# Kernel optimization log

Measured on AMD Instinct MI355X. Metric: run time of the kernel, lower is better.

## Reference

```python
import jax, jax.numpy as jnp
import numpy as np

B, H, W, D = 4, 64, 64, 384
M, P = 12, 9
DH = D // M             # 32 head dim
DFF = 3 * D             # 1152 FFN hidden
N = H * W               # 4096 queries (single level)


def setup_inputs():
    key = jax.random.key(0)
    ks = jax.random.split(key, 12)
    g = lambda k, s, sc=0.02: jax.random.normal(k, s, jnp.float32) * sc
    return {
        "x": jax.random.normal(ks[0], (B, D, H, W), jnp.float32),
        "qry_masks": jnp.zeros((B, H, W), jnp.float32),
        "so_w": g(ks[1], (M * P * 2, D)), "so_b": g(ks[2], (M * P * 2,)),
        "aw_w": g(ks[3], (M * P, D)), "aw_b": g(ks[4], (M * P,)),
        "vp_w": g(ks[5], (D, D)), "vp_b": jnp.zeros((D,), jnp.float32),
        "op_w": g(ks[6], (D, D)), "op_b": jnp.zeros((D,), jnp.float32),
        "ln1_g": jnp.ones((D,), jnp.float32), "ln1_b": jnp.zeros((D,), jnp.float32),
        "w1": g(ks[7], (DFF, D)), "w2": g(ks[8], (D, DFF)),
        "ln2_g": jnp.ones((D,), jnp.float32), "ln2_b": jnp.zeros((D,), jnp.float32),
        "level_embed": g(ks[9], (1, D), 1.0),
    }


def _layernorm(x, g, b, eps=1e-5):
    mu = x.mean(-1, keepdims=True)
    v = ((x - mu) ** 2).mean(-1, keepdims=True)
    return (x - mu) * jax.lax.rsqrt(v + eps) * g + b


def _sine_pos(mask):
    # mask: [B,H,W] bool. mmdet SinePositionalEncoding(num_feats=D//2, normalize=True)
    not_mask = (~mask).astype(jnp.float32)
    y = jnp.cumsum(not_mask, 1)
    x = jnp.cumsum(not_mask, 2)
    eps, scale = 1e-6, 2.0 * np.pi
    y = y / (y[:, -1:, :] + eps) * scale
    x = x / (x[:, :, -1:] + eps) * scale
    nf = D // 2
    dim_t = 10000.0 ** (2.0 * (jnp.arange(nf) // 2).astype(jnp.float32) / nf)
    px, py = x[..., None] / dim_t, y[..., None] / dim_t

    def interleave(p):
        return jnp.stack([jnp.sin(p[..., 0::2]), jnp.cos(p[..., 1::2])], -1).reshape(p.shape[:-1] + (nf,))

    return jnp.concatenate([interleave(py), interleave(px)], -1)  # [B,H,W,D]


def _bilinear_gather(v, px, py):
    # v: [B,M,HW,DH]; px,py: [B,M,NP] pixel coords (grid_sample align_corners=False, zero pad)
    x0 = jnp.floor(px); y0 = jnp.floor(py)
    lx, ly = px - x0, py - y0
    x0i, y0i = x0.astype(jnp.int32), y0.astype(jnp.int32)
    out = jnp.zeros(v.shape[:2] + (px.shape[-1], v.shape[-1]), v.dtype)
    for dx, dy, wgt in ((0, 0, (1 - lx) * (1 - ly)), (1, 0, lx * (1 - ly)),
                        (0, 1, (1 - lx) * ly), (1, 1, lx * ly)):
        xi, yi = x0i + dx, y0i + dy
        valid = ((xi >= 0) & (xi < W) & (yi >= 0) & (yi < H)).astype(v.dtype)
        idx = jnp.clip(yi, 0, H - 1) * W + jnp.clip(xi, 0, W - 1)
        g = jnp.take_along_axis(v, idx[..., None], axis=2)  # [B,M,NP,DH]
        out = out + (wgt * valid)[..., None] * g
    return out


def _msdeform_attn(q, value_in, ref, mask_flat,
                   so_w, so_b, aw_w, aw_b, vp_w, vp_b, op_w, op_b):
    value = value_in @ vp_w.T + vp_b                      # [B,N,D]
    value = jnp.where(mask_flat[..., None], 0.0, value)
    so = (q @ so_w.T + so_b).reshape(B, N, M, P, 2)       # single level
    aw = jax.nn.softmax((q @ aw_w.T + aw_b).reshape(B, N, M, P), axis=-1)
    norm = jnp.array([W, H], jnp.float32)
    loc = ref[:, :, None, None, :] + so / norm            # [B,N,M,P,2] in [0,1]
    v = value.reshape(B, N, M, DH).transpose(0, 2, 1, 3)  # [B,M,HW,DH]
    px = (loc[..., 0] * W - 0.5).transpose(0, 2, 1, 3).reshape(B, M, N * P)
    py = (loc[..., 1] * H - 0.5).transpose(0, 2, 1, 3).reshape(B, M, N * P)
    sampled = _bilinear_gather(v, px, py).reshape(B, M, N, P, DH)
    out = jnp.einsum('bmnpd,bnmp->bnmd', sampled, aw).reshape(B, N, D)
    return out @ op_w.T + op_b


def reference(x, qry_masks, so_w, so_b, aw_w, aw_b, vp_w, vp_b, op_w, op_b,
              ln1_g, ln1_b, w1, w2, ln2_g, ln2_b, level_embed):
    mask = (qry_masks == 255.0)                           # [B,H,W] bool
    pos = _sine_pos(mask).reshape(B, N, D) + level_embed[0]
    src = x.reshape(B, D, N).transpose(0, 2, 1)           # [B,N,D]
    mask_flat = mask.reshape(B, N)
    gy, gx = jnp.meshgrid((jnp.arange(H, dtype=jnp.float32) + 0.5) / H,
                          (jnp.arange(W, dtype=jnp.float32) + 0.5) / W, indexing='ij')
    ref = jnp.stack([gx.reshape(-1), gy.reshape(-1)], -1)[None]  # [1,N,2] (x,y)
    q = src
    attn = _msdeform_attn(q + pos, q, ref, mask_flat,
                          so_w, so_b, aw_w, aw_b, vp_w, vp_b, op_w, op_b)
    q = _layernorm(q + attn, ln1_g, ln1_b)
    q = _layernorm(q + jax.nn.relu(q @ w1.T) @ w2.T, ln2_g, ln2_b)
    return q.transpose(0, 2, 1).reshape(B, D, H, W)
```

## Files before the change

kernel.cpp:

```cpp
#include <hip/hip_runtime.h>
#include <math.h>

#define Bc   4
#define Hc   64
#define Wc   64
#define Dc   384
#define Nc   4096
#define Mc   12
#define Pc   9
#define DHc  32
#define DFFc 1152
#define BNc  (Bc*Nc)

typedef __attribute__((ext_vector_type(8))) short short8;
typedef __attribute__((ext_vector_type(4))) float floatx4;

__device__ __forceinline__ ushort f2bf(float f) {
    union { float f; unsigned u; } v; v.f = f;
    unsigned r = v.u + 0x7fffu + ((v.u >> 16) & 1u);
    return (ushort)(r >> 16);
}
__device__ __forceinline__ float bf2f(ushort u) {
    union { unsigned u; float f; } v; v.u = (unsigned)u << 16; return v.f;
}

__device__ __forceinline__ void gload_lds16(const void* g, void* l) {
    __builtin_amdgcn_global_load_lds(
        (const __attribute__((address_space(1))) void*)(uintptr_t)g,
        (__attribute__((address_space(3))) void*)(uintptr_t)l,
        16, 0, 0);
}

#define SOW_N  82944
#define AWW_N  41472
#define VPW_N  147456
#define OPW_N  147456
#define W1_N   442368
#define W2_N   442368
#define WTOT   1304064

__global__ void init_kernel(const float* __restrict__ so_w,
                            const float* __restrict__ aw_w,
                            const float* __restrict__ vp_w,
                            const float* __restrict__ op_w,
                            const float* __restrict__ w1,
                            const float* __restrict__ w2,
                            const float* __restrict__ so_b,
                            const float* __restrict__ aw_b,
                            ushort* __restrict__ out,
                            float* __restrict__ bias_out) {
    int i = blockIdx.x * 256 + threadIdx.x;
    if (i < WTOT) {
        float v;
        int j = i;
        if (j < SOW_N) v = so_w[j];
        else if ((j -= SOW_N) < AWW_N) v = aw_w[j];
        else if ((j -= AWW_N) < VPW_N) v = vp_w[j];
        else if ((j -= VPW_N) < OPW_N) v = op_w[j];
        else if ((j -= OPW_N) < W1_N)  v = w1[j];
        else { j -= W1_N; v = w2[j]; }
        out[i] = f2bf(v);
        return;
    }
    int j = i - WTOT;
    if (j < 384) {
        bias_out[j] = (j < 216) ? so_b[j] : (j < 324 ? aw_b[j - 216] : 0.f);
    }
}

__global__ __launch_bounds__(256) void cumsum_kernel(
        const float* __restrict__ qmask,
        float* __restrict__ cum_y, float* __restrict__ cum_x) {
    __shared__ float nm[64 * 65];
    __shared__ float ot[64 * 65];
    int b = blockIdx.x;
    int t = threadIdx.x;
    const float* qm = qmask + b * 4096;
    #pragma unroll
    for (int k = 0; k < 16; ++k) {
        int idx = t + k * 256;
        nm[(idx >> 6) * 65 + (idx & 63)] = (qm[idx] == 255.0f) ? 0.f : 1.f;
    }
    __syncthreads();
    if (t < 64) {
        float run = 0.f;
        for (int h = 0; h < 64; ++h) { run += nm[h * 65 + t]; ot[h * 65 + t] = run; }
    }
    __syncthreads();
    #pragma unroll
    for (int k = 0; k < 16; ++k) {
        int idx = t + k * 256;
        cum_y[b * 4096 + idx] = ot[(idx >> 6) * 65 + (idx & 63)];
    }
    __syncthreads();
    if (t < 64) {
        float run = 0.f;
        for (int w = 0; w < 64; ++w) { run += nm[t * 65 + w]; ot[t * 65 + w] = run; }
    }
    __syncthreads();
    #pragma unroll
    for (int k = 0; k < 16; ++k) {
        int idx = t + k * 256;
        cum_x[b * 4096 + idx] = ot[(idx >> 6) * 65 + (idx & 63)];
    }
}

__global__ void transpose_pos_kernel(const float* __restrict__ x,
                                     const float* __restrict__ cum_y,
                                     const float* __restrict__ cum_x,
                                     const float* __restrict__ level_embed,
                                     ushort* __restrict__ src_bf,
                                     ushort* __restrict__ qpos_bf) {
    __shared__ float tile[32][33];
    int b  = blockIdx.z;
    int n0 = blockIdx.x * 32, d0 = blockIdx.y * 32;
    int tx = threadIdx.x, ty = threadIdx.y;
    tile[ty][tx] = x[((size_t)b * Dc + (d0 + ty)) * Nc + (n0 + tx)];
    __syncthreads();
    int n = n0 + ty, d = d0 + tx;
    float v = tile[tx][ty];
    size_t oi = ((size_t)b * Nc + n) * Dc + d;
    src_bf[oi] = f2bf(v);
    int h = n >> 6, w = n & 63;
    const float TWO_PI = 6.28318530717958647692f;
    float vy = cum_y[(b * Hc + h) * Wc + w] /
               (cum_y[(b * Hc + (Hc - 1)) * Wc + w] + 1e-6f) * TWO_PI;
    float vx = cum_x[(b * Hc + h) * Wc + w] /
               (cum_x[(b * Hc + h) * Wc + (Wc - 1)] + 1e-6f) * TWO_PI;
    int   i  = (d < 192) ? d : d - 192;
    float vv = (d < 192) ? vy : vx;
    float e   = (float)(i >> 1) * (2.0f / 192.0f);
    float idt = exp2f(e * -13.28771237954945f);
    float ang = vv * idt;
    float pe  = (i & 1) ? __cosf(ang) : __sinf(ang);
    qpos_bf[oi] = f2bf(v + pe + level_embed[d]);
}

template <int KT>
__device__ __forceinline__ void gemm_core(
        const ushort* __restrict__ A, const ushort* __restrict__ Wt,
        const float* __restrict__ bias,
        float* __restrict__ Cf, ushort* __restrict__ Cb,
        int Nout, int relu, const float* __restrict__ qmask,
        ushort* As, ushort* Bs) {
    constexpr int NCH = KT / 32;
    const int tid  = threadIdx.x;
    const int m0   = blockIdx.x * 128;
    const int n0   = blockIdx.y * 128;
    const int lane = tid & 63;
    const int wv   = tid >> 6;
    const int wr   = (wv >> 1) * 64;
    const int wc   = (wv & 1) * 64;
    const int quad = lane >> 4;
    const int lrow = lane & 15;
    const int srow = wv * 32 + (lane >> 2);
    const int scol = (lane & 3) * 8;

    floatx4 acc[4][4];
    #pragma unroll
    for (int i = 0; i < 4; ++i)
        #pragma unroll
        for (int j = 0; j < 4; ++j)
            acc[i][j] = (floatx4)(0.f);

    #pragma unroll
    for (int s = 0; s < 2; ++s) {
        gload_lds16(A  + (size_t)(m0 + srow + s * 16) * KT + scol,
                    As + wv * 1024 + s * 512);
        gload_lds16(Wt + (size_t)(n0 + srow + s * 16) * KT + scol,
                    Bs + wv * 1024 + s * 512);
    }

    for (int c = 0; c < NCH; ++c) {
        const int cur = c & 1;
        __syncthreads();
        if (c + 1 < NCH) {
            const int k0 = (c + 1) * 32;
            #pragma unroll
            for (int s = 0; s < 2; ++s) {
                gload_lds16(A  + (size_t)(m0 + srow + s * 16) * KT + k0 + scol,
                            As + (cur ^ 1) * 4096 + wv * 1024 + s * 512);
                gload_lds16(Wt + (size_t)(n0 + srow + s * 16) * KT + k0 + scol,
                            Bs + (cur ^ 1) * 4096 + wv * 1024 + s * 512);
            }
        }
        short8 afr[4], bfr[4];
        #pragma unroll
        for (int i = 0; i < 4; ++i)
            afr[i] = *(const short8*)(As + cur * 4096 +
                                      (wr + i * 16 + lrow) * 32 + quad * 8);
        #pragma unroll
        for (int j = 0; j < 4; ++j)
            bfr[j] = *(const short8*)(Bs + cur * 4096 +
                                      (wc + j * 16 + lrow) * 32 + quad * 8);
        #pragma unroll
        for (int i = 0; i < 4; ++i)
            #pragma unroll
            for (int j = 0; j < 4; ++j)
                acc[i][j] = __builtin_amdgcn_mfma_f32_16x16x32_bf16(
                    afr[i], bfr[j], acc[i][j], 0, 0, 0);
    }

    float mz[4][4];
    #pragma unroll
    for (int i = 0; i < 4; ++i)
        #pragma unroll
        for (int r = 0; r < 4; ++r) {
            int row = m0 + wr + i * 16 + quad * 4 + r;
            mz[i][r] = (qmask && qmask[row] == 255.0f) ? 0.f : 1.f;
        }

    #pragma unroll
    for (int i = 0; i < 4; ++i) {
        #pragma unroll
        for (int j = 0; j < 4; ++j) {
            int col = n0 + wc + j * 16 + lrow;
            if (col >= Nout) continue;
            float bsv = bias ? bias[col] : 0.f;
            #pragma unroll
            for (int r = 0; r < 4; ++r) {
                int row = m0 + wr + i * 16 + quad * 4 + r;
                float v = acc[i][j][r] + bsv;
                if (relu) v = fmaxf(v, 0.f);
                v *= mz[i][r];
                if (Cf) Cf[(size_t)row * Nout + col] = v;
                if (Cb) Cb[(size_t)row * Nout + col] = f2bf(v);
            }
        }
    }
}

__global__ __launch_bounds__(256) void gemm_dual_kernel(
        const ushort* __restrict__ A0, const ushort* __restrict__ W0,
        const float* __restrict__ b0, float* __restrict__ Cf0,
        const ushort* __restrict__ A1, const ushort* __restrict__ W1,
        const float* __restrict__ b1, ushort* __restrict__ Cb1,
        const float* __restrict__ qmask) {
    __shared__ ushort As[2 * 128 * 32];
    __shared__ ushort Bs[2 * 128 * 32];
    if (blockIdx.z == 0)
        gemm_core<384>(A0, W0, b0, Cf0, nullptr, 384, 0, nullptr, As, Bs);
    else
        gemm_core<384>(A1, W1, b1, nullptr, Cb1, 384, 0, qmask, As, Bs);
}

template <int KT>
__global__ __launch_bounds__(512) void gemm_fullrow_kernel(
        const ushort* __restrict__ A, const ushort* __restrict__ Wt,
        const float* __restrict__ bias, const void* __restrict__ resid,
        const float* __restrict__ g, const float* __restrict__ beta,
        float* __restrict__ outf, ushort* __restrict__ outb) {
    constexpr int NCH = KT / 32;
    __shared__ ushort As[4 * 2048];
    __shared__ ushort Bs[4 * 12288];
    __shared__ float eps1[8][64], eps2[8][64];
    __shared__ float mu_l[64], rs_l[64];
    const int tid  = threadIdx.x;
    const int lane = tid & 63;
    const int wv   = tid >> 6;
    const int quad = lane >> 4;
    const int lrow = lane & 15;
    const int m0   = blockIdx.x * 64;
    const int srow = lane >> 2;
    const int scol = (lane & 3) * 8;

    floatx4 acc[4][3];
    #pragma unroll
    for (int i = 0; i < 4; ++i)
        #pragma unroll
        for (int j = 0; j < 3; ++j)
            acc[i][j] = (floatx4)(0.f);

#define STAGE_CHUNK(c, buf)                                                   \
    {   const int k0_ = (c) * 32;                                             \
        if (wv < 4)                                                           \
            gload_lds16(A + (size_t)(m0 + wv * 16 + srow) * KT + k0_ + scol,  \
                        As + (buf) * 2048 + wv * 512);                        \
        _Pragma("unroll")                                                     \
        for (int s_ = 0; s_ < 3; ++s_)                                        \
            gload_lds16(Wt + (size_t)(wv * 48 + s_ * 16 + srow) * KT + k0_ + scol, \
                        Bs + (buf) * 12288 + wv * 1536 + s_ * 512);           \
    }

    STAGE_CHUNK(0, 0)
    STAGE_CHUNK(1, 1)
    STAGE_CHUNK(2, 2)

    #pragma unroll
    for (int c = 0; c < NCH; ++c) {
        const int rem = (NCH - 1 - c) >= 2 ? 2 : (NCH - 1 - c);
        if (wv < 4) {
            if (rem == 2)      asm volatile("s_waitcnt vmcnt(8)" ::: "memory");
            else if (rem == 1) asm volatile("s_waitcnt vmcnt(4)" ::: "memory");
            else               asm volatile("s_waitcnt vmcnt(0)" ::: "memory");
        } else {
            if (rem == 2)      asm volatile("s_waitcnt vmcnt(6)" ::: "memory");
            else if (rem == 1) asm volatile("s_waitcnt vmcnt(3)" ::: "memory");
            else               asm volatile("s_waitcnt vmcnt(0)" ::: "memory");
        }
        __builtin_amdgcn_s_barrier();
        __builtin_amdgcn_sched_barrier(0);
        if (c + 3 < NCH) { STAGE_CHUNK(c + 3, (c + 3) & 3) }
        const int buf = c & 3;
        short8 afr[4], bfr[3];
        #pragma unroll
        for (int i = 0; i < 4; ++i)
            afr[i] = *(const short8*)(As + buf * 2048 +
                                      (i * 16 + lrow) * 32 + quad * 8);
        #pragma unroll
        for (int j = 0; j < 3; ++j)
            bfr[j] = *(const short8*)(Bs + buf * 12288 +
                                      (wv * 48 + j * 16 + lrow) * 32 + quad * 8);
        #pragma unroll
        for (int i = 0; i < 4; ++i)
            #pragma unroll
            for (int j = 0; j < 3; ++j)
                acc[i][j] = __builtin_amdgcn_mfma_f32_16x16x32_bf16(
                    afr[i], bfr[j], acc[i][j], 0, 0, 0);
    }
#undef STAGE_CHUNK

    float s1[16], s2[16];
    #pragma unroll
    for (int k = 0; k < 16; ++k) { s1[k] = 0.f; s2[k] = 0.f; }
    #pragma unroll
    for (int i = 0; i < 4; ++i) {
        #pragma unroll
        for (int r = 0; r < 4; ++r) {
            int rl = i * 16 + quad * 4 + r;
            #pragma unroll
            for (int j = 0; j < 3; ++j) {
                int col = wv * 48 + j * 16 + lrow;
                float t = acc[i][j][r];
                if (bias) t += bias[col];
                t += bf2f(((const ushort*)resid)[(size_t)(m0 + rl) * Dc + col]);
                acc[i][j][r] = t;
                s1[i * 4 + r] += t;
                s2[i * 4 + r] += t * t;
            }
        }
    }
    #pragma unroll
    for (int mm = 1; mm < 16; mm <<= 1) {
        #pragma unroll
        for (int k = 0; k < 16; ++k) {
            s1[k] += __shfl_xor(s1[k], mm);
            s2[k] += __shfl_xor(s2[k], mm);
        }
    }
    if (lrow == 0) {
        #pragma unroll
        for (int i = 0; i < 4; ++i)
            #pragma unroll
            for (int r = 0; r < 4; ++r) {
                int rl = i * 16 + quad * 4 + r;
                eps1[wv][rl] = s1[i * 4 + r];
                eps2[wv][rl] = s2[i * 4 + r];
            }
    }
    __syncthreads();
    if (tid < 64) {
        float a1 = 0.f, a2 = 0.f;
        #pragma unroll
        for (int w = 0; w < 8; ++w) { a1 += eps1[w][tid]; a2 += eps2[w][tid]; }
        float mu  = a1 * (1.0f / Dc);
        float var = a2 * (1.0f / Dc) - mu * mu;
        mu_l[tid] = mu;
        rs_l[tid] = rsqrtf(var + 1e-5f);
    }
    __syncthreads();
    #pragma unroll
    for (int i = 0; i < 4; ++i) {
        #pragma unroll
        for (int r = 0; r < 4; ++r) {
            int rl = i * 16 + quad * 4 + r;
            float mu = mu_l[rl], rs = rs_l[rl];
            #pragma unroll
            for (int j = 0; j < 3; ++j) {
                int col = wv * 48 + j * 16 + lrow;
                float v = (acc[i][j][r] - mu) * rs * g[col] + beta[col];
                outf[(size_t)(m0 + rl) * Dc + col] = v;
                outb[(size_t)(m0 + rl) * Dc + col] = f2bf(v);
            }
        }
    }
}

__global__ __launch_bounds__(512) void ffn_fused_kernel(
        const ushort* __restrict__ A,
        const ushort* __restrict__ W1b,
        const ushort* __restrict__ W2b,
        const float* __restrict__ resid,
        const float* __restrict__ g, const float* __restrict__ beta,
        float* __restrict__ outf) {
    __shared__ ushort smem[69632];
    ushort* Ast = smem;
    ushort* Hs  = smem + 24576;
    ushort* W1s = smem + 32768;
    ushort* W2s = smem + 45056;
    __shared__ float eps1[8][64], eps2[8][64];
    __shared__ float mu_l[64], rs_l[64];

    const int tid  = threadIdx.x;
    const int lane = tid & 63;
    const int wv   = tid >> 6;
    const int quad = lane >> 4;
    const int lrow = lane & 15;
    const int m0   = blockIdx.x * 64;
    const int srow = lane >> 2;
    const int scol = (lane & 3) * 8;

    ushort* W1w = W1s + wv * 1536;
    ushort* W2w = W2s + wv * 3072;

    floatx4 acc2[4][3];
    #pragma unroll
    for (int i = 0; i < 4; ++i)
        #pragma unroll
        for (int j = 0; j < 3; ++j)
            acc2[i][j] = (floatx4)(0.f);

#define STAGE_W1(hcv, kcv, buf)                                               \
    gload_lds16(W1b + (size_t)((hcv) * 128 + wv * 16 + srow) * 384 + (kcv) * 32 + scol, \
                W1w + (buf) * 512 + lane * 8);

#define STAGE_W2(hcv, kc2v, buf)                                              \
    _Pragma("unroll")                                                         \
    for (int s_ = 0; s_ < 3; ++s_)                                            \
        gload_lds16(W2b + (size_t)(wv * 48 + s_ * 16 + srow) * 1152 + (hcv) * 128 + (kc2v) * 32 + scol, \
                    W2w + (buf) * 1536 + s_ * 512 + lane * 8);

    #pragma unroll
    for (int k = 0; k < 6; ++k) {
        int l   = tid + 512 * k;
        int kc_ = l >> 8;
        int rem = l & 255;
        gload_lds16(A + (size_t)(m0 + (rem >> 2)) * 384 + kc_ * 32 + (rem & 3) * 8,
                    Ast + l * 8);
    }
    STAGE_W1(0, 0, 0)
    STAGE_W1(0, 1, 1)
    asm volatile("s_waitcnt vmcnt(2)" ::: "memory");
    __builtin_amdgcn_sched_barrier(0);
    __builtin_amdgcn_s_barrier();
    __builtin_amdgcn_sched_barrier(0);

    floatx4 acc1[4];
    for (int hc = 0; hc < 9; ++hc) {
        #pragma unroll
        for (int i = 0; i < 4; ++i) acc1[i] = (floatx4)(0.f);

        #pragma unroll
        for (int kc = 0; kc < 12; ++kc) {
            if (kc < 10)      { STAGE_W1(hc, kc + 2, (kc + 2) % 3) }
            else if (kc == 10){ STAGE_W2(hc, 0, 0) }
            else              { STAGE_W2(hc, 1, 1) }
            if (kc < 10)       asm volatile("s_waitcnt vmcnt(2)" ::: "memory");
            else if (kc == 10) asm volatile("s_waitcnt vmcnt(4)" ::: "memory");
            else               asm volatile("s_waitcnt vmcnt(6)" ::: "memory");
            short8 afr[4], bfr;
            #pragma unroll
            for (int i = 0; i < 4; ++i)
                afr[i] = *(const short8*)(Ast + kc * 2048 +
                                          (i * 16 + lrow) * 32 + quad * 8);
            bfr = *(const short8*)(W1w + (kc % 3) * 512 + lrow * 32 + quad * 8);
            #pragma unroll
            for (int i = 0; i < 4; ++i)
                acc1[i] = __builtin_amdgcn_mfma_f32_16x16x32_bf16(
                    afr[i], bfr, acc1[i], 0, 0, 0);
        }

        #pragma unroll
        for (int i = 0; i < 4; ++i)
            #pragma unroll
            for (int r = 0; r < 4; ++r) {
                int row = i * 16 + quad * 4 + r;
                Hs[(wv >> 1) * 2048 + row * 32 + (wv & 1) * 16 + lrow] =
                    f2bf(fmaxf(acc1[i][r], 0.f));
            }
        asm volatile("s_waitcnt lgkmcnt(0)" ::: "memory");
        __builtin_amdgcn_sched_barrier(0);
        __builtin_amdgcn_s_barrier();
        __builtin_amdgcn_sched_barrier(0);

        #pragma unroll
        for (int kc2 = 0; kc2 < 4; ++kc2) {
            if (kc2 == 0)      asm volatile("s_waitcnt vmcnt(3)" ::: "memory");
            else if (kc2 == 1) asm volatile("s_waitcnt vmcnt(4)" ::: "memory");
            else if (kc2 == 2) asm volatile("s_waitcnt vmcnt(5)" ::: "memory");
            else               asm volatile("s_waitcnt vmcnt(1)" ::: "memory");
            short8 afr[4], bfr[3];
            #pragma unroll
            for (int i = 0; i < 4; ++i)
                afr[i] = *(const short8*)(Hs + kc2 * 2048 +
                                          (i * 16 + lrow) * 32 + quad * 8);
            #pragma unroll
            for (int j = 0; j < 3; ++j)
                bfr[j] = *(const short8*)(W2w + (kc2 & 1) * 1536 +
                                          (j * 16 + lrow) * 32 + quad * 8);
            asm volatile("s_waitcnt lgkmcnt(0)" ::: "memory");
            __builtin_amdgcn_sched_barrier(0);
            if (kc2 == 0)      { STAGE_W2(hc, 2, 0) STAGE_W1(hc + 1, 0, 0) }
            else if (kc2 == 1) { STAGE_W2(hc, 3, 1) STAGE_W1(hc + 1, 1, 1) }
            #pragma unroll
            for (int i = 0; i < 4; ++i)
                #pragma unroll
                for (int j = 0; j < 3; ++j)
                    acc2[i][j] = __builtin_amdgcn_mfma_f32_16x16x32_bf16(
                        afr[i], bfr[j], acc2[i][j], 0, 0, 0);
        }
        asm volatile("s_waitcnt lgkmcnt(0)" ::: "memory");
        __builtin_amdgcn_sched_barrier(0);
        __builtin_amdgcn_s_barrier();
        __builtin_amdgcn_sched_barrier(0);
    }
    asm volatile("s_waitcnt vmcnt(0)" ::: "memory");
#undef STAGE_W1
#undef STAGE_W2

    float s1[16], s2[16];
    #pragma unroll
    for (int k = 0; k < 16; ++k) { s1[k] = 0.f; s2[k] = 0.f; }
    #pragma unroll
    for (int i = 0; i < 4; ++i) {
        #pragma unroll
        for (int r = 0; r < 4; ++r) {
            int rl = i * 16 + quad * 4 + r;
            #pragma unroll
            for (int j = 0; j < 3; ++j) {
                int col = wv * 48 + j * 16 + lrow;
                float t = acc2[i][j][r];
                t += resid[(size_t)(m0 + rl) * Dc + col];
                acc2[i][j][r] = t;
                s1[i * 4 + r] += t;
                s2[i * 4 + r] += t * t;
            }
        }
    }
    #pragma unroll
    for (int mm = 1; mm < 16; mm <<= 1) {
        #pragma unroll
        for (int k = 0; k < 16; ++k) {
            s1[k] += __shfl_xor(s1[k], mm);
            s2[k] += __shfl_xor(s2[k], mm);
        }
    }
    if (lrow == 0) {
        #pragma unroll
        for (int i = 0; i < 4; ++i)
            #pragma unroll
            for (int r = 0; r < 4; ++r) {
                int rl = i * 16 + quad * 4 + r;
                eps1[wv][rl] = s1[i * 4 + r];
                eps2[wv][rl] = s2[i * 4 + r];
            }
    }
    __syncthreads();
    if (tid < 64) {
        float a1 = 0.f, a2 = 0.f;
        #pragma unroll
        for (int w = 0; w < 8; ++w) { a1 += eps1[w][tid]; a2 += eps2[w][tid]; }
        float mu  = a1 * (1.0f / Dc);
        float var = a2 * (1.0f / Dc) - mu * mu;
        mu_l[tid] = mu;
        rs_l[tid] = rsqrtf(var + 1e-5f);
    }
    __syncthreads();
    #pragma unroll
    for (int i = 0; i < 4; ++i) {
        #pragma unroll
        for (int r = 0; r < 4; ++r) {
            int rl = i * 16 + quad * 4 + r;
            float mu = mu_l[rl], rs = rs_l[rl];
            #pragma unroll
            for (int j = 0; j < 3; ++j) {
                int col = wv * 48 + j * 16 + lrow;
                acc2[i][j][r] = (acc2[i][j][r] - mu) * rs * g[col] + beta[col];
            }
        }
    }
    float* tile = (float*)smem;
    const int b   = m0 >> 12;
    const int n0r = m0 & 4095;
    #pragma unroll
    for (int gp = 0; gp < 2; ++gp) {
        __syncthreads();
        if ((wv >> 2) == gp) {
            int cbase = (wv & 3) * 48;
            #pragma unroll
            for (int i = 0; i < 4; ++i)
                #pragma unroll
                for (int j = 0; j < 3; ++j) {
                    int c = cbase + j * 16 + lrow;
                    #pragma unroll
                    for (int r = 0; r < 4; ++r) {
                        int rl = i * 16 + quad * 4 + r;
                        tile[rl * 193 + c] = acc2[i][j][r];
                    }
                }
        }
        __syncthreads();
        const int row = tid & 63;
        const int cp  = tid >> 6;
        #pragma unroll
        for (int it = 0; it < 24; ++it) {
            int c = it * 8 + cp;
            outf[((size_t)(b * Dc + gp * 192 + c)) * Nc + n0r + row] =
                tile[row * 193 + c];
        }
    }
}

__global__ __launch_bounds__(256) void deform_attn_kernel(
        const ushort* __restrict__ value_bf, const float* __restrict__ soaw,
        ushort* __restrict__ out) {
    int bid   = blockIdx.x;
    int slice = bid % 48;
    int h     = bid / 48;
    int m  = slice % Mc;
    int b  = slice / Mc;
    int w  = threadIdx.x >> 2;
    int l4 = threadIdx.x & 3;
    int n  = (h << 6) | w;
    int bn = b * Nc + n;
    const float* sop = soaw + (size_t)bn * 384 + m * 18;
    const float* lgt = soaw + (size_t)bn * 384 + 216 + m * Pc;
    float awv[Pc];
    float mx = lgt[0];
    #pragma unroll
    for (int i = 1; i < Pc; ++i) mx = fmaxf(mx, lgt[i]);
    float ssum = 0.f;
    #pragma unroll
    for (int i = 0; i < Pc; ++i) { awv[i] = __expf(lgt[i] - mx); ssum += awv[i]; }
    float sinv = 1.f / ssum;
    const ushort* vb = value_bf + ((size_t)b * Nc) * Dc + m * DHc + l4 * 8;
    float acc[8] = {0.f, 0.f, 0.f, 0.f, 0.f, 0.f, 0.f, 0.f};
    #pragma unroll
    for (int p = 0; p < Pc; ++p) {
        float2 so2 = *(const float2*)(sop + p * 2);
        float px = (float)w + so2.x;
        float py = (float)h + so2.y;
        float x0f = floorf(px), y0f = floorf(py);
        float lx = px - x0f, ly = py - y0f;
        int x0 = (int)x0f, y0 = (int)y0f;
        int x1 = x0 + 1,  y1 = y0 + 1;
        float a = awv[p] * sinv;
        float w00 = (1.f - lx) * (1.f - ly) * a;
        float w01 = lx * (1.f - ly) * a;
        float w10 = (1.f - lx) * ly * a;
        float w11 = lx * ly * a;
        bool bx0 = (unsigned)x0 < 64u, bx1 = (unsigned)x1 < 64u;
        bool by0 = (unsigned)y0 < 64u, by1 = (unsigned)y1 < 64u;
        w00 = (bx0 && by0) ? w00 : 0.f;
        w01 = (bx1 && by0) ? w01 : 0.f;
        w10 = (bx0 && by1) ? w10 : 0.f;
        w11 = (bx1 && by1) ? w11 : 0.f;
        int cx0 = min(max(x0, 0), 63), cx1 = min(max(x1, 0), 63);
        int cy0 = min(max(y0, 0), 63), cy1 = min(max(y1, 0), 63);
        uint4 q00 = *(const uint4*)(vb + (size_t)(cy0 * 64 + cx0) * Dc);
        uint4 q01 = *(const uint4*)(vb + (size_t)(cy0 * 64 + cx1) * Dc);
        uint4 q10 = *(const uint4*)(vb + (size_t)(cy1 * 64 + cx0) * Dc);
        uint4 q11 = *(const uint4*)(vb + (size_t)(cy1 * 64 + cx1) * Dc);
        union { unsigned u; float f; } t;
        #define ACC2(word, wg, k)                                   \
            t.u = (word) << 16;         acc[k]     += (wg) * t.f;   \
            t.u = (word) & 0xffff0000u; acc[k + 1] += (wg) * t.f;
        #define ACC8(q, wg) \
            ACC2((q).x, wg, 0) ACC2((q).y, wg, 2) ACC2((q).z, wg, 4) ACC2((q).w, wg, 6)
        ACC8(q00, w00) ACC8(q01, w01) ACC8(q10, w10) ACC8(q11, w11)
        #undef ACC8
        #undef ACC2
    }
    short8 o;
    #pragma unroll
    for (int k = 0; k < 8; ++k) o[k] = (short)f2bf(acc[k]);
    *(short8*)(out + (size_t)bn * Dc + m * DHc + l4 * 8) = o;
}

extern "C" void kernel_launch(void* const* d_in, const int* in_sizes, int n_in,
                              void* d_out, int out_size, void* d_ws, size_t ws_size,
                              hipStream_t stream) {
    (void)in_sizes; (void)n_in; (void)out_size; (void)ws_size;
    const float* x      = (const float*)d_in[0];
    const float* qmask  = (const float*)d_in[1];
    const float* so_w   = (const float*)d_in[2];
    const float* so_b   = (const float*)d_in[3];
    const float* aw_w   = (const float*)d_in[4];
    const float* aw_b   = (const float*)d_in[5];
    const float* vp_w   = (const float*)d_in[6];
    const float* vp_b   = (const float*)d_in[7];
    const float* op_w   = (const float*)d_in[8];
    const float* op_b   = (const float*)d_in[9];
    const float* ln1_g  = (const float*)d_in[10];
    const float* ln1_b  = (const float*)d_in[11];
    const float* w1     = (const float*)d_in[12];
    const float* w2     = (const float*)d_in[13];
    const float* ln2_g  = (const float*)d_in[14];
    const float* ln2_b  = (const float*)d_in[15];
    const float* lvl    = (const float*)d_in[16];
    float* out = (float*)d_out;

    float*  ws       = (float*)d_ws;
    float*  q1_f     = ws;
    ushort* src_bf   = (ushort*)(q1_f + 6291456);
    ushort* qpos_bf  = src_bf + 6291456;
    ushort* value_bf = qpos_bf + 6291456;
    ushort* hbuf_bf  = value_bf + 6291456;
    float*  soaw_f   = (float*)hbuf_bf;
    ushort* wbuf     = hbuf_bf + 18874368;
    float*  soaw_bias= (float*)(wbuf + 1304064);
    float*  cum_y    = soaw_bias + 384;
    float*  cum_x    = cum_y + 16384;

    const ushort* soaw_wb = wbuf;
    const ushort* vp_wb = soaw_wb + SOW_N + AWW_N;
    const ushort* op_wb = vp_wb + VPW_N;
    const ushort* w1_b  = op_wb + OPW_N;
    const ushort* w2_b  = w1_b + W1_N;

    init_kernel<<<(WTOT + 384 + 255) / 256, 256, 0, stream>>>(
        so_w, aw_w, vp_w, op_w, w1, w2, so_b, aw_b, wbuf, soaw_bias);
    cumsum_kernel<<<Bc, 256, 0, stream>>>(qmask, cum_y, cum_x);
    transpose_pos_kernel<<<dim3(Nc / 32, Dc / 32, Bc), dim3(32, 32), 0, stream>>>(
        x, cum_y, cum_x, lvl, src_bf, qpos_bf);
    gemm_dual_kernel<<<dim3(BNc / 128, 3, 2), 256, 0, stream>>>(
        qpos_bf, soaw_wb, soaw_bias, soaw_f,
        src_bf, vp_wb, vp_b, value_bf, qmask);
    deform_attn_kernel<<<3072, 256, 0, stream>>>(
        value_bf, soaw_f, qpos_bf);
    gemm_fullrow_kernel<384><<<BNc / 64, 512, 0, stream>>>(
        qpos_bf, op_wb, op_b, src_bf, ln1_g, ln1_b, q1_f, qpos_bf);
    ffn_fused_kernel<<<BNc / 64, 512, 0, stream>>>(
        qpos_bf, w1_b, w2_b, q1_f, ln2_g, ln2_b, out);
}
```

Baseline: 259.4 us.

## Deepen W1 prefetch to four buffers and vectorize swizzled hidden-tile stores

The fused FFN kernel's W1 staging ring grows from three to four LDS buffers, so weight tiles are prefetched one k-step further ahead, and the vmcnt waits and W2 staging slots are shifted to match. The first GEMM swaps its MFMA operands so each lane holds a row's four contiguous hidden values. These are packed into one 8-byte LDS store to an XOR-swizzled slot instead of four scalar 2-byte stores, and the second GEMM reads back through the same swizzle. The aims are to hide global-load latency and to cut LDS store count and bank conflicts, at the cost of more LDS per block and harder-to-check wait counts.

```diff
diff --git a/kernel.cpp b/kernel.cpp
--- a/kernel.cpp
+++ b/kernel.cpp
@@ -13,6 +13,7 @@
 #define BNc  (Bc*Nc)
 
 typedef __attribute__((ext_vector_type(8))) short short8;
+typedef __attribute__((ext_vector_type(4))) short short4v;
 typedef __attribute__((ext_vector_type(4))) float floatx4;
 
 __device__ __forceinline__ ushort f2bf(float f) {
@@ -393,11 +394,11 @@
         const float* __restrict__ resid,
         const float* __restrict__ g, const float* __restrict__ beta,
         float* __restrict__ outf) {
-    __shared__ ushort smem[69632];
+    __shared__ ushort smem[73728];
     ushort* Ast = smem;
     ushort* Hs  = smem + 24576;
     ushort* W1s = smem + 32768;
-    ushort* W2s = smem + 45056;
+    ushort* W2s = smem + 49152;
     __shared__ float eps1[8][64], eps2[8][64];
     __shared__ float mu_l[64], rs_l[64];
 
@@ -410,7 +411,7 @@
     const int srow = lane >> 2;
     const int scol = (lane & 3) * 8;
 
-    ushort* W1w = W1s + wv * 1536;
+    ushort* W1w = W1s + wv * 2048;
     ushort* W2w = W2s + wv * 3072;
 
     floatx4 acc2[4][3];
@@ -440,7 +441,8 @@
     }
     STAGE_W1(0, 0, 0)
     STAGE_W1(0, 1, 1)
-    asm volatile("s_waitcnt vmcnt(2)" ::: "memory");
+    STAGE_W1(0, 2, 2)
+    asm volatile("s_waitcnt vmcnt(3)" ::: "memory");
     __builtin_amdgcn_sched_barrier(0);
     __builtin_amdgcn_s_barrier();
     __builtin_amdgcn_sched_barrier(0);
@@ -452,32 +454,35 @@
 
         #pragma unroll
         for (int kc = 0; kc < 12; ++kc) {
-            if (kc < 10)      { STAGE_W1(hc, kc + 2, (kc + 2) % 3) }
-            else if (kc == 10){ STAGE_W2(hc, 0, 0) }
-            else              { STAGE_W2(hc, 1, 1) }
-            if (kc < 10)       asm volatile("s_waitcnt vmcnt(2)" ::: "memory");
-            else if (kc == 10) asm volatile("s_waitcnt vmcnt(4)" ::: "memory");
+            if (kc <= 8)       { STAGE_W1(hc, kc + 3, (kc + 3) & 3) }
+            else if (kc == 9)  { STAGE_W2(hc, 0, 0) }
+            else if (kc == 10) { STAGE_W2(hc, 1, 1) }
+            if (kc <= 8)       asm volatile("s_waitcnt vmcnt(3)" ::: "memory");
+            else if (kc == 9)  asm volatile("s_waitcnt vmcnt(5)" ::: "memory");
+            else if (kc == 10) asm volatile("s_waitcnt vmcnt(7)" ::: "memory");
             else               asm volatile("s_waitcnt vmcnt(6)" ::: "memory");
             short8 afr[4], bfr;
             #pragma unroll
             for (int i = 0; i < 4; ++i)
                 afr[i] = *(const short8*)(Ast + kc * 2048 +
                                           (i * 16 + lrow) * 32 + quad * 8);
-            bfr = *(const short8*)(W1w + (kc % 3) * 512 + lrow * 32 + quad * 8);
+            bfr = *(const short8*)(W1w + (kc & 3) * 512 + lrow * 32 + quad * 8);
             #pragma unroll
             for (int i = 0; i < 4; ++i)
                 acc1[i] = __builtin_amdgcn_mfma_f32_16x16x32_bf16(
-                    afr[i], bfr, acc1[i], 0, 0, 0);
-        }
-
-        #pragma unroll
-        for (int i = 0; i < 4; ++i)
-            #pragma unroll
-            for (int r = 0; r < 4; ++r) {
-                int row = i * 16 + quad * 4 + r;
-                Hs[(wv >> 1) * 2048 + row * 32 + (wv & 1) * 16 + lrow] =
-                    f2bf(fmaxf(acc1[i][r], 0.f));
-            }
+                    bfr, afr[i], acc1[i], 0, 0, 0);
+        }
+
+        #pragma unroll
+        for (int i = 0; i < 4; ++i) {
+            short4v pk;
+            #pragma unroll
+            for (int r = 0; r < 4; ++r)
+                pk[r] = (short)f2bf(fmaxf(acc1[i][r], 0.f));
+            int mrow = i * 16 + lrow;
+            int slot = ((wv & 1) * 4 + quad) ^ (mrow & 6);
+            *(short4v*)(Hs + (wv >> 1) * 2048 + mrow * 32 + slot * 4) = pk;
+        }
         asm volatile("s_waitcnt lgkmcnt(0)" ::: "memory");
         __builtin_amdgcn_sched_barrier(0);
         __builtin_amdgcn_s_barrier();
@@ -488,12 +493,14 @@
             if (kc2 == 0)      asm volatile("s_waitcnt vmcnt(3)" ::: "memory");
             else if (kc2 == 1) asm volatile("s_waitcnt vmcnt(4)" ::: "memory");
             else if (kc2 == 2) asm volatile("s_waitcnt vmcnt(5)" ::: "memory");
-            else               asm volatile("s_waitcnt vmcnt(1)" ::: "memory");
+            else               asm volatile("s_waitcnt vmcnt(2)" ::: "memory");
             short8 afr[4], bfr[3];
             #pragma unroll
-            for (int i = 0; i < 4; ++i)
-                afr[i] = *(const short8*)(Hs + kc2 * 2048 +
-                                          (i * 16 + lrow) * 32 + quad * 8);
+            for (int i = 0; i < 4; ++i) {
+                int mrow = i * 16 + lrow;
+                int s0 = (quad * 2) ^ (mrow & 6);
+                afr[i] = *(const short8*)(Hs + kc2 * 2048 + mrow * 32 + s0 * 4);
+            }
             #pragma unroll
             for (int j = 0; j < 3; ++j)
                 bfr[j] = *(const short8*)(W2w + (kc2 & 1) * 1536 +
@@ -502,6 +509,7 @@
             __builtin_amdgcn_sched_barrier(0);
             if (kc2 == 0)      { STAGE_W2(hc, 2, 0) STAGE_W1(hc + 1, 0, 0) }
             else if (kc2 == 1) { STAGE_W2(hc, 3, 1) STAGE_W1(hc + 1, 1, 1) }
+            else if (kc2 == 2) { STAGE_W1(hc + 1, 2, 2) }
             #pragma unroll
             for (int i = 0; i < 4; ++i)
                 #pragma unroll
```

After: 254.2 us. 1.02x faster.
